# Performance work log

Hardware: AMD Instinct MI355X
Metric: run time of the kernel (lower is better)

## Reference

```python
import jax, jax.numpy as jnp
import numpy as np

B, S, D, H, F = 2, 2048, 1024, 16, 4096
DH = D // H  # per-head dim = 64
EPS = 1e-5


def _layer_norm(x, g, b):
    mu = jnp.mean(x, axis=-1, keepdims=True)
    var = jnp.mean((x - mu) ** 2, axis=-1, keepdims=True)
    return (x - mu) * jax.lax.rsqrt(var + EPS) * g + b


def _mha(q_in, kv_in, wq, bq, wk, bk, wv, bv, wo, bo, causal):
    b, s, d = q_in.shape
    q = (q_in @ wq + bq).reshape(b, s, H, DH).transpose(0, 2, 1, 3)
    k = (kv_in @ wk + bk).reshape(b, s, H, DH).transpose(0, 2, 1, 3)
    v = (kv_in @ wv + bv).reshape(b, s, H, DH).transpose(0, 2, 1, 3)
    scores = jnp.einsum('bhqd,bhkd->bhqk', q, k) / np.sqrt(DH).astype(np.float32)
    if causal:
        mask = jnp.tril(jnp.ones((s, s), dtype=bool))
        scores = jnp.where(mask, scores, -jnp.inf)
    attn = jax.nn.softmax(scores, axis=-1)
    out = jnp.einsum('bhqk,bhkd->bhqd', attn, v)
    out = out.transpose(0, 2, 1, 3).reshape(b, s, d)
    return out @ wo + bo


def setup_inputs() -> dict:
    key = jax.random.key(0)
    ks = iter(jax.random.split(key, 24))
    def w(shape, fan_in):
        return jax.random.normal(next(ks), shape, jnp.float32) / np.sqrt(fan_in).astype(np.float32)
    inp = {
        'encoder_output': jax.random.normal(next(ks), (B, S, D), jnp.float32),
        'decoder_input': jax.random.normal(next(ks), (B, S, D), jnp.float32),
    }
    for pre in ('sa', 'ca'):
        for nm in ('wq', 'wk', 'wv', 'wo'):
            inp[f'{pre}_{nm}'] = w((D, D), D)
            inp[f'{pre}_b{nm[-1]}'] = jnp.zeros((D,), jnp.float32)
        inp[f'{pre}_g'] = jnp.ones((D,), jnp.float32)
        inp[f'{pre}_bt'] = jnp.zeros((D,), jnp.float32)
    inp['f_w1'] = w((D, F), D); inp['f_b1'] = jnp.zeros((F,), jnp.float32)
    inp['f_w2'] = w((F, D), F); inp['f_b2'] = jnp.zeros((D,), jnp.float32)
    inp['f_g'] = jnp.ones((D,), jnp.float32); inp['f_bt'] = jnp.zeros((D,), jnp.float32)
    return inp


def reference(encoder_output, decoder_input,
              sa_wq, sa_bq, sa_wk, sa_bk, sa_wv, sa_bv, sa_wo, sa_bo, sa_g, sa_bt,
              ca_wq, ca_bq, ca_wk, ca_bk, ca_wv, ca_bv, ca_wo, ca_bo, ca_g, ca_bt,
              f_w1, f_b1, f_w2, f_b2, f_g, f_bt):
    # masked self-attention + residual + LN
    x = _mha(decoder_input, decoder_input, sa_wq, sa_bq, sa_wk, sa_bk, sa_wv, sa_bv, sa_wo, sa_bo, True)
    x = _layer_norm(x + decoder_input, sa_g, sa_bt)
    # encoder-decoder attention + residual + LN
    y = _mha(x, encoder_output, ca_wq, ca_bq, ca_wk, ca_bk, ca_wv, ca_bv, ca_wo, ca_bo, False)
    y = _layer_norm(y + x, ca_g, ca_bt)
    # FFN + residual + LN
    h = jax.nn.relu(y @ f_w1 + f_b1) @ f_w2 + f_b2
    return _layer_norm(h + y, f_g, f_bt)
```

## Files before the change

kernel.cpp:

```cpp
#include <hip/hip_runtime.h>
#include <hip/hip_bf16.h>


typedef __attribute__((ext_vector_type(8))) short bf16x8;
typedef __attribute__((ext_vector_type(4))) float f32x4;

#define LOG2E 1.44269504088896340736f

constexpr int Bb = 2, Ss = 2048, Dd = 1024, Hh = 16, DHd = 64, Ff = 4096;
constexpr int Mrows = Bb * Ss;
constexpr int BHS = Bb * Hh * Ss;

static __device__ __forceinline__ ushort f2b(float f) {
    union { float f; unsigned u; } x{f};
    unsigned r = x.u + 0x7fffu + ((x.u >> 16) & 1u);
    return (ushort)(r >> 16);
}

static __device__ __forceinline__ unsigned pk2(float a, float b) {
    __hip_bfloat162 h = __float22bfloat162_rn(make_float2(a, b));
    unsigned u;
    __builtin_memcpy(&u, &h, 4);
    return u;
}

static __device__ __forceinline__ unsigned pk2t(float a, float b) {
    union { float f; unsigned u; } ua{a}, ub{b};
    return __builtin_amdgcn_perm(ub.u, ua.u, 0x07060302);
}

static __device__ __forceinline__ void gl2lds16(const void* g, void* l) {
    __builtin_amdgcn_global_load_lds(
        (const __attribute__((address_space(1))) void*)g,
        (__attribute__((address_space(3))) void*)l, 16, 0, 0);
}

__global__ __launch_bounds__(256) void cvt_kernel(const float* __restrict__ in,
                                                  ushort* __restrict__ out) {
    int i = (blockIdx.x * 256 + threadIdx.x) * 4;
    float4 v = *(const float4*)(in + i);
    ushort4 u;
    u.x = f2b(v.x); u.y = f2b(v.y); u.z = f2b(v.z); u.w = f2b(v.w);
    *(ushort4*)(out + i) = u;
}

__global__ __launch_bounds__(256) void wtrans_kernel(const float* __restrict__ w,
                                                     ushort* __restrict__ wT,
                                                     int K, int N) {
    __shared__ float t[32][33];
    int tx = threadIdx.x & 31, ty = threadIdx.x >> 5;
    int kb = blockIdx.y * 32, nb = blockIdx.x * 32;
#pragma unroll
    for (int i = 0; i < 4; i++)
        t[ty + i * 8][tx] = w[(size_t)(kb + ty + i * 8) * N + nb + tx];
    __syncthreads();
#pragma unroll
    for (int i = 0; i < 4; i++)
        wT[(size_t)(nb + ty + i * 8) * K + kb + tx] = f2b(t[tx][ty + i * 8]);
}

__global__ __launch_bounds__(256) void pack_bias(const float* __restrict__ a,
                                                 const float* __restrict__ b,
                                                 const float* __restrict__ c,
                                                 float* __restrict__ out) {
    int i = blockIdx.x * 256 + threadIdx.x;
    const float* src = a; int j = i;
    if (i >= 2048)      { src = c; j = i - 2048; }
    else if (i >= 1024) { src = b; j = i - 1024; }
    out[i] = src[j];
}

__global__ __launch_bounds__(256) void gemm_kernel(const ushort* __restrict__ A,
                                                   const ushort* __restrict__ BT,
                                                   const float* __restrict__ bias,
                                                   void* __restrict__ out,
                                                   int M, int N, int K, int klen,
                                                   int mode, int relu, float qsc,
                                                   int vwhich) {
    __shared__ __align__(16) ushort As[128 * 64];
    __shared__ __align__(16) ushort Bs[128 * 64];
    const int tid = threadIdx.x;
    const int lane = tid & 63, wave = tid >> 6;
    const int lr = lane & 15, quad = lane >> 4;
    const int wm = wave & 1, wn = wave >> 1;
    const int m0 = blockIdx.y * 128, n0 = blockIdx.x * 128;
    const int kz = blockIdx.z;
    const int kstart = kz * klen;

    f32x4 acc[4][4];
#pragma unroll
    for (int i = 0; i < 4; i++)
#pragma unroll
        for (int j = 0; j < 4; j++) acc[i][j] = (f32x4){0.f, 0.f, 0.f, 0.f};

    const int srow = tid >> 3;
    const int gchunk = ((tid & 7) ^ (srow & 7)) * 8;
    const ushort* aBase = A + (size_t)(m0 + srow) * K + gchunk;
    const ushort* bBase = BT + (size_t)(n0 + srow) * K + gchunk;
    const size_t rowStep = (size_t)32 * K;

    const int slotA = ((quad) ^ (lr & 7)) * 8;
    const int slotB = ((4 + quad) ^ (lr & 7)) * 8;

    for (int k0 = kstart; k0 < kstart + klen; k0 += 64) {
#pragma unroll
        for (int c = 0; c < 4; c++) {
            gl2lds16(aBase + c * rowStep + k0, &As[c * 2048 + tid * 8]);
            gl2lds16(bBase + c * rowStep + k0, &Bs[c * 2048 + tid * 8]);
        }
        __syncthreads();
#pragma unroll
        for (int kk = 0; kk < 2; kk++) {
            const int slot = kk ? slotB : slotA;
            bf16x8 af[4], bfr[4];
#pragma unroll
            for (int i = 0; i < 4; i++)
                af[i] = *(const bf16x8*)&As[(wm * 64 + i * 16 + lr) * 64 + slot];
#pragma unroll
            for (int j = 0; j < 4; j++)
                bfr[j] = *(const bf16x8*)&Bs[(wn * 64 + j * 16 + lr) * 64 + slot];
#pragma unroll
            for (int i = 0; i < 4; i++)
#pragma unroll
                for (int j = 0; j < 4; j++)
                    acc[i][j] = __builtin_amdgcn_mfma_f32_16x16x32_bf16(af[i], bfr[j], acc[i][j], 0, 0, 0);
        }
        __syncthreads();
    }

#pragma unroll
    for (int j = 0; j < 4; j++) {
        int col = n0 + wn * 64 + j * 16 + lr;
        float bv = (bias && kz == 0) ? bias[col] : 0.f;
#pragma unroll
        for (int i = 0; i < 4; i++) {
            int row0 = m0 + wm * 64 + i * 16 + quad * 4;
            float v[4];
#pragma unroll
            for (int r = 0; r < 4; r++) {
                v[r] = acc[i][j][r] + bv;
                if (relu) v[r] = fmaxf(v[r], 0.f);
            }
            if (mode == 0) {
                float* op = (float*)out + (size_t)kz * M * N;
#pragma unroll
                for (int r = 0; r < 4; r++)
                    op[(size_t)(row0 + r) * N + col] = v[r];
            } else if (mode == 1) {
#pragma unroll
                for (int r = 0; r < 4; r++)
                    ((ushort*)out)[(size_t)(row0 + r) * N + col] = f2b(v[r]);
            } else {
                int which = col >> 10, n1 = col & 1023;
                int h = n1 >> 6, dh = n1 & 63;
                int b = row0 >> 11, s0 = row0 & 2047;
                size_t wbase = (size_t)which * (Bb * Hh * Ss * DHd);
                if (which == vwhich) {
                    uint2 pk;
                    pk.x = pk2(v[0], v[1]); pk.y = pk2(v[2], v[3]);
                    *(uint2*)((ushort*)out + wbase +
                              ((size_t)(b * Hh + h) * DHd + dh) * Ss + s0) = pk;
                } else {
                    float sc = (which == 0) ? qsc : 1.f;
#pragma unroll
                    for (int r = 0; r < 4; r++)
                        ((ushort*)out)[wbase + (((size_t)(b * Hh + h) * Ss + s0 + r) * DHd) + dh] =
                            f2b(v[r] * sc);
                }
            }
        }
    }
}

__global__ __launch_bounds__(256, 5) void attn_kernel(const ushort* __restrict__ Q,
                                                      const ushort* __restrict__ Kg,
                                                      const ushort* __restrict__ VT,
                                                      float* __restrict__ Op0,
                                                      float* __restrict__ Op1,
                                                      float* __restrict__ Ml,
                                                      int causal) {
    __shared__ ushort Ks[64][72];
    __shared__ ushort Vs[64][72];
    __shared__ ushort Ps[4][16][72];
    const int tid = threadIdx.x;
    const int lane = tid & 63, w = tid >> 6;
    const int lr = lane & 15, quad = lane >> 4;
    const int p = blockIdx.z;
    const int qt = causal ? (gridDim.x - 1 - blockIdx.x) : blockIdx.x;
    const int bh = blockIdx.y;
    const size_t hb = (size_t)bh * Ss * DHd;
    const int qrow = qt * 64 + w * 16;
    const int qg = qrow + lr;

    bf16x8 qf0 = *(const bf16x8*)(Q + hb + (size_t)qg * DHd + quad * 8);
    bf16x8 qf1 = *(const bf16x8*)(Q + hb + (size_t)qg * DHd + 32 + quad * 8);

    f32x4 o[4];
#pragma unroll
    for (int d = 0; d < 4; d++) o[d] = (f32x4){0.f, 0.f, 0.f, 0.f};
    float l_i = 0.f;

    const int srow = tid >> 3, sseg = tid & 7;

    const int ktEnd = causal ? (qt + 1) : (Ss / 64);
    for (int kt = p; kt < ktEnd; kt += 2) {
        const int k0 = kt * 64;
#pragma unroll
        for (int io = 0; io < 2; io++) {
            *(bf16x8*)&Ks[srow + io * 32][sseg * 8] =
                *(const bf16x8*)(Kg + hb + (size_t)(k0 + srow + io * 32) * DHd + sseg * 8);
            *(bf16x8*)&Vs[srow + io * 32][sseg * 8] =
                *(const bf16x8*)(VT + hb + (size_t)(srow + io * 32) * Ss + k0 + sseg * 8);
        }
        __syncthreads();

        f32x4 st[4];
#pragma unroll
        for (int k16 = 0; k16 < 4; k16++) {
            bf16x8 a0 = *(const bf16x8*)&Ks[k16 * 16 + lr][quad * 8];
            bf16x8 a1 = *(const bf16x8*)&Ks[k16 * 16 + lr][32 + quad * 8];
            f32x4 z = (f32x4){0.f, 0.f, 0.f, 0.f};
            z = __builtin_amdgcn_mfma_f32_16x16x32_bf16(a0, qf0, z, 0, 0, 0);
            st[k16] = __builtin_amdgcn_mfma_f32_16x16x32_bf16(a1, qf1, z, 0, 0, 0);
        }
        if (causal && kt == qt) {
#pragma unroll
            for (int k16 = 0; k16 < 4; k16++)
#pragma unroll
                for (int r = 0; r < 4; r++) {
                    int key = k0 + k16 * 16 + quad * 4 + r;
                    if (key > qg) st[k16][r] = -1e30f;
                }
        }
        float pv[4][4], psum = 0.f;
#pragma unroll
        for (int k16 = 0; k16 < 4; k16++)
#pragma unroll
            for (int r = 0; r < 4; r++) {
                pv[k16][r] = __builtin_amdgcn_exp2f(fminf(st[k16][r], 88.f));
                psum += pv[k16][r];
            }
        psum += __shfl_xor(psum, 16);
        psum += __shfl_xor(psum, 32);
        l_i += psum;
#pragma unroll
        for (int k16 = 0; k16 < 4; k16++) {
            uint2 pk;
            pk.x = pk2t(pv[k16][0], pv[k16][1]);
            pk.y = pk2t(pv[k16][2], pv[k16][3]);
            *(uint2*)&Ps[w][lr][k16 * 16 + quad * 4] = pk;
        }
#pragma unroll
        for (int kh = 0; kh < 2; kh++) {
            bf16x8 pb = *(const bf16x8*)&Ps[w][lr][kh * 32 + quad * 8];
#pragma unroll
            for (int dt = 0; dt < 4; dt++) {
                bf16x8 av = *(const bf16x8*)&Vs[dt * 16 + lr][kh * 32 + quad * 8];
                o[dt] = __builtin_amdgcn_mfma_f32_16x16x32_bf16(av, pb, o[dt], 0, 0, 0);
            }
        }
        __syncthreads();
    }

    float* Op = p ? Op1 : Op0;
    if (quad == 0)
        Ml[(size_t)p * BHS + (size_t)bh * Ss + qg] = l_i;
    size_t ob = ((size_t)bh * Ss + qg) * 64;
#pragma unroll
    for (int dt = 0; dt < 4; dt++)
        *(f32x4*)(Op + ob + dt * 16 + quad * 4) = o[dt];
}

__global__ __launch_bounds__(256) void attn_combine(const float* __restrict__ Op0,
                                                    const float* __restrict__ Op1,
                                                    const float* __restrict__ Ml,
                                                    ushort* __restrict__ O) {
    int g = blockIdx.x * 256 + threadIdx.x;
    int q = g >> 4, seg = g & 15;
    float inv = 1.f / (Ml[q] + Ml[BHS + q]);
    f32x4 x = *(const f32x4*)(Op0 + (size_t)q * 64 + seg * 4);
    f32x4 y = *(const f32x4*)(Op1 + (size_t)q * 64 + seg * 4);
    int bh = q >> 11, sq = q & 2047, bb = bh >> 4, h = bh & 15;
    uint2 u;
    u.x = pk2((x[0] + y[0]) * inv, (x[1] + y[1]) * inv);
    u.y = pk2((x[2] + y[2]) * inv, (x[3] + y[3]) * inv);
    *(uint2*)(O + ((size_t)(bb * Ss + sq)) * Dd + h * 64 + seg * 4) = u;
}

__global__ __launch_bounds__(256) void ln_kernel(const float* __restrict__ a0,
                                                 const float* __restrict__ a1,
                                                 const float* __restrict__ a2,
                                                 const float* __restrict__ a3,
                                                 const float* __restrict__ resid,
                                                 const float* __restrict__ g,
                                                 const float* __restrict__ bt,
                                                 float* __restrict__ out32,
                                                 ushort* __restrict__ outb) {
    const int row = blockIdx.x, tid = threadIdx.x;
    const size_t base = (size_t)row * Dd + tid * 4;
    float4 av = *(const float4*)(a0 + base);
    if (a1) { float4 t = *(const float4*)(a1 + base); av.x += t.x; av.y += t.y; av.z += t.z; av.w += t.w; }
    if (a2) { float4 t = *(const float4*)(a2 + base); av.x += t.x; av.y += t.y; av.z += t.z; av.w += t.w; }
    if (a3) { float4 t = *(const float4*)(a3 + base); av.x += t.x; av.y += t.y; av.z += t.z; av.w += t.w; }
    float4 rv = *(const float4*)(resid + base);
    float x0 = av.x + rv.x, x1 = av.y + rv.y, x2 = av.z + rv.z, x3 = av.w + rv.w;
    float s = x0 + x1 + x2 + x3;
    float q = x0 * x0 + x1 * x1 + x2 * x2 + x3 * x3;
#pragma unroll
    for (int off = 1; off <= 32; off <<= 1) {
        s += __shfl_xor(s, off);
        q += __shfl_xor(q, off);
    }
    __shared__ float red[8];
    int wave = tid >> 6, lane = tid & 63;
    if (lane == 0) { red[wave] = s; red[4 + wave] = q; }
    __syncthreads();
    s = red[0] + red[1] + red[2] + red[3];
    q = red[4] + red[5] + red[6] + red[7];
    float mu = s * (1.f / Dd);
    float var = q * (1.f / Dd) - mu * mu;
    float rs = rsqrtf(var + 1e-5f);
    int col = tid * 4;
    float4 gv = *(const float4*)(g + col);
    float4 bv = *(const float4*)(bt + col);
    float y0 = (x0 - mu) * rs * gv.x + bv.x;
    float y1 = (x1 - mu) * rs * gv.y + bv.y;
    float y2 = (x2 - mu) * rs * gv.z + bv.z;
    float y3 = (x3 - mu) * rs * gv.w + bv.w;
    if (out32) *(float4*)(out32 + base) = make_float4(y0, y1, y2, y3);
    if (outb) {
        ushort4 u; u.x = f2b(y0); u.y = f2b(y1); u.z = f2b(y2); u.w = f2b(y3);
        *(ushort4*)(outb + base) = u;
    }
}

constexpr size_t OFF_XB     = 0;
constexpr size_t OFF_ENCB   = OFF_XB     + 8388608;
constexpr size_t OFF_QKVWT  = OFF_ENCB   + 8388608;
constexpr size_t OFF_CAWQT  = OFF_QKVWT  + 6291456;
constexpr size_t OFF_CAKVT  = OFF_CAWQT  + 2097152;
constexpr size_t OFF_SAWOT  = OFF_CAKVT  + 4194304;
constexpr size_t OFF_CAWOT  = OFF_SAWOT  + 2097152;
constexpr size_t OFF_FW1T   = OFF_CAWOT  + 2097152;
constexpr size_t OFF_FW2T   = OFF_FW1T   + 8388608;
constexpr size_t OFF_SABQKV = OFF_FW2T   + 8388608;
constexpr size_t OFF_CABKV  = OFF_SABQKV + 12288;
constexpr size_t OFF_QB     = OFF_CABKV  + 8192;
constexpr size_t OFF_KB     = OFF_QB     + 8388608;
constexpr size_t OFF_VB     = OFF_KB     + 8388608;
constexpr size_t OFF_ATTNO  = OFF_VB     + 8388608;
constexpr size_t OFF_F1     = OFF_ATTNO  + 8388608;
constexpr size_t OFF_F2     = OFF_F1     + 16777216;
constexpr size_t OFF_X1B    = OFF_F2     + 16777216;
constexpr size_t OFF_F3     = OFF_X1B    + 8388608;
constexpr size_t OFF_YB     = OFF_F3     + 16777216;
constexpr size_t OFF_H1B    = OFF_YB     + 8388608;

extern "C" void kernel_launch(void* const* d_in, const int* in_sizes, int n_in,
                              void* d_out, int out_size, void* d_ws, size_t ws_size,
                              hipStream_t stream) {
    const float* enc   = (const float*)d_in[0];
    const float* dec   = (const float*)d_in[1];
    const float* sa_wq = (const float*)d_in[2];
    const float* sa_bq = (const float*)d_in[3];
    const float* sa_wk = (const float*)d_in[4];
    const float* sa_bk = (const float*)d_in[5];
    const float* sa_wv = (const float*)d_in[6];
    const float* sa_bv = (const float*)d_in[7];
    const float* sa_wo = (const float*)d_in[8];
    const float* sa_bo = (const float*)d_in[9];
    const float* sa_g  = (const float*)d_in[10];
    const float* sa_bt = (const float*)d_in[11];
    const float* ca_wq = (const float*)d_in[12];
    const float* ca_bq = (const float*)d_in[13];
    const float* ca_wk = (const float*)d_in[14];
    const float* ca_bk = (const float*)d_in[15];
    const float* ca_wv = (const float*)d_in[16];
    const float* ca_bv = (const float*)d_in[17];
    const float* ca_wo = (const float*)d_in[18];
    const float* ca_bo = (const float*)d_in[19];
    const float* ca_g  = (const float*)d_in[20];
    const float* ca_bt = (const float*)d_in[21];
    const float* f_w1  = (const float*)d_in[22];
    const float* f_b1  = (const float*)d_in[23];
    const float* f_w2  = (const float*)d_in[24];
    const float* f_b2  = (const float*)d_in[25];
    const float* f_g   = (const float*)d_in[26];
    const float* f_bt  = (const float*)d_in[27];

    char* ws = (char*)d_ws;
    ushort* xb     = (ushort*)(ws + OFF_XB);
    ushort* encb   = (ushort*)(ws + OFF_ENCB);
    ushort* qkvwT  = (ushort*)(ws + OFF_QKVWT);
    ushort* cawqT  = (ushort*)(ws + OFF_CAWQT);
    ushort* cakvT  = (ushort*)(ws + OFF_CAKVT);
    ushort* sawoT  = (ushort*)(ws + OFF_SAWOT);
    ushort* cawoT  = (ushort*)(ws + OFF_CAWOT);
    ushort* fw1T   = (ushort*)(ws + OFF_FW1T);
    ushort* fw2T   = (ushort*)(ws + OFF_FW2T);
    float*  sabqkv = (float*)(ws + OFF_SABQKV);
    float*  cabkv  = (float*)(ws + OFF_CABKV);
    ushort* qb     = (ushort*)(ws + OFF_QB);
    ushort* kb     = (ushort*)(ws + OFF_KB);
    ushort* vbt    = (ushort*)(ws + OFF_VB);
    ushort* attno  = (ushort*)(ws + OFF_ATTNO);
    float*  f1     = (float*)(ws + OFF_F1);
    float*  f2     = (float*)(ws + OFF_F2);
    ushort* x1b    = (ushort*)(ws + OFF_X1B);
    float*  x1f    = (float*)(ws + OFF_F3);
    ushort* yb     = (ushort*)(ws + OFF_YB);
    ushort* h1b    = (ushort*)(ws + OFF_H1B);
    float*  yfp    = (float*)(ws + OFF_QB);
    float*  ml     = (float*)(ws + OFF_H1B);

    const float QSC = 0.125f * LOG2E;
    const size_t MN = (size_t)Mrows * Dd;

    cvt_kernel<<<4096, 256, 0, stream>>>(dec, xb);
    cvt_kernel<<<4096, 256, 0, stream>>>(enc, encb);
    dim3 tgDD(32, 32);
    wtrans_kernel<<<tgDD, 256, 0, stream>>>(sa_wq, qkvwT,                 Dd, Dd);
    wtrans_kernel<<<tgDD, 256, 0, stream>>>(sa_wk, qkvwT + 1024 * 1024,   Dd, Dd);
    wtrans_kernel<<<tgDD, 256, 0, stream>>>(sa_wv, qkvwT + 2 * 1024 * 1024, Dd, Dd);
    wtrans_kernel<<<tgDD, 256, 0, stream>>>(sa_wo, sawoT,                 Dd, Dd);
    wtrans_kernel<<<tgDD, 256, 0, stream>>>(ca_wq, cawqT,                 Dd, Dd);
    wtrans_kernel<<<tgDD, 256, 0, stream>>>(ca_wk, cakvT,                 Dd, Dd);
    wtrans_kernel<<<tgDD, 256, 0, stream>>>(ca_wv, cakvT + 1024 * 1024,   Dd, Dd);
    wtrans_kernel<<<tgDD, 256, 0, stream>>>(ca_wo, cawoT,                 Dd, Dd);
    wtrans_kernel<<<dim3(128, 32), 256, 0, stream>>>(f_w1, fw1T, Dd, Ff);
    wtrans_kernel<<<dim3(32, 128), 256, 0, stream>>>(f_w2, fw2T, Ff, Dd);
    pack_bias<<<12, 256, 0, stream>>>(sa_bq, sa_bk, sa_bv, sabqkv);
    pack_bias<<<8, 256, 0, stream>>>(ca_bk, ca_bv, nullptr, cabkv);

    gemm_kernel<<<dim3(24, 32, 1), 256, 0, stream>>>(xb, qkvwT, sabqkv, qb,
                                                     Mrows, 3072, Dd, Dd, 2, 0, QSC, 2);
    attn_kernel<<<dim3(32, 32, 2), 256, 0, stream>>>(qb, kb, vbt, f1, x1f, ml, 1);
    attn_combine<<<4096, 256, 0, stream>>>(f1, x1f, ml, attno);
    gemm_kernel<<<dim3(8, 32, 2), 256, 0, stream>>>(attno, sawoT, sa_bo, f1,
                                                    Mrows, Dd, Dd, 512, 0, 0, 1.f, -1);
    ln_kernel<<<4096, 256, 0, stream>>>(f1, f2, nullptr, nullptr, dec,
                                        sa_g, sa_bt, x1f, x1b);

    gemm_kernel<<<dim3(8, 32, 1), 256, 0, stream>>>(x1b, cawqT, ca_bq, qb,
                                                    Mrows, Dd, Dd, Dd, 2, 0, QSC, -1);
    gemm_kernel<<<dim3(16, 32, 1), 256, 0, stream>>>(encb, cakvT, cabkv, kb,
                                                     Mrows, 2048, Dd, Dd, 2, 0, 1.f, 1);
    attn_kernel<<<dim3(32, 32, 2), 256, 0, stream>>>(qb, kb, vbt, f1, f2, ml, 0);
    attn_combine<<<4096, 256, 0, stream>>>(f1, f2, ml, attno);
    gemm_kernel<<<dim3(8, 32, 2), 256, 0, stream>>>(attno, cawoT, ca_bo, f1,
                                                    Mrows, Dd, Dd, 512, 0, 0, 1.f, -1);
    ln_kernel<<<4096, 256, 0, stream>>>(f1, f2, nullptr, nullptr, x1f,
                                        ca_g, ca_bt, yfp, yb);

    gemm_kernel<<<dim3(32, 32, 1), 256, 0, stream>>>(yb, fw1T, f_b1, h1b,
                                                     Mrows, Ff, Dd, Dd, 1, 1, 1.f, -1);
    gemm_kernel<<<dim3(8, 32, 4), 256, 0, stream>>>(h1b, fw2T, f_b2, f1,
                                                    Mrows, Dd, Ff, 1024, 0, 0, 1.f, -1);
    ln_kernel<<<4096, 256, 0, stream>>>(f1, f1 + MN, f1 + 2 * MN, f1 + 3 * MN, yfp,
                                        f_g, f_bt, (float*)d_out, nullptr);
}
```

Baseline: 619.3 us.

## Rewrite attention with 256-row query tiles and 32x32x16 MFMA, register-resident P

The attention kernel now handles 256 query rows per block, 64 per wave, instead of 64. It uses 32x32x16 bf16 MFMAs and keeps the probability tile in registers via v_permlane32_swap instead of staging it through LDS. K/V tiles are loaded with direct global-to-LDS copies into an XOR-swizzled layout, and causal split blocks are paired in reverse order to balance work. The goal is more K/V reuse per LDS load and fewer LDS round trips, at the cost of more registers, lower occupancy (launch bound 2) and a 4x smaller grid.

```diff
diff --git a/kernel.cpp b/kernel.cpp
--- a/kernel.cpp
+++ b/kernel.cpp
@@ -4,6 +4,7 @@
 
 typedef __attribute__((ext_vector_type(8))) short bf16x8;
 typedef __attribute__((ext_vector_type(4))) float f32x4;
+typedef __attribute__((ext_vector_type(16))) float f32x16;
 
 #define LOG2E 1.44269504088896340736f
 
@@ -172,103 +173,142 @@
     }
 }
 
-__global__ __launch_bounds__(256, 5) void attn_kernel(const ushort* __restrict__ Q,
+__global__ __launch_bounds__(256, 2) void attn_kernel(const ushort* __restrict__ Q,
                                                       const ushort* __restrict__ Kg,
                                                       const ushort* __restrict__ VT,
                                                       float* __restrict__ Op0,
                                                       float* __restrict__ Op1,
                                                       float* __restrict__ Ml,
                                                       int causal) {
-    __shared__ ushort Ks[64][72];
-    __shared__ ushort Vs[64][72];
-    __shared__ ushort Ps[4][16][72];
+    __shared__ __align__(16) ushort Ks[64 * 64];
+    __shared__ __align__(16) ushort Vs[64 * 64];
     const int tid = threadIdx.x;
     const int lane = tid & 63, w = tid >> 6;
-    const int lr = lane & 15, quad = lane >> 4;
+    const int lr31 = lane & 31, hi = lane >> 5, l7 = lane & 7;
+    const int hi4 = hi * 4;
     const int p = blockIdx.z;
-    const int qt = causal ? (gridDim.x - 1 - blockIdx.x) : blockIdx.x;
+    const int qt = causal ? (p ? blockIdx.x : (gridDim.x - 1 - blockIdx.x))
+                          : blockIdx.x;
     const int bh = blockIdx.y;
     const size_t hb = (size_t)bh * Ss * DHd;
-    const int qrow = qt * 64 + w * 16;
-    const int qg = qrow + lr;
-
-    bf16x8 qf0 = *(const bf16x8*)(Q + hb + (size_t)qg * DHd + quad * 8);
-    bf16x8 qf1 = *(const bf16x8*)(Q + hb + (size_t)qg * DHd + 32 + quad * 8);
-
-    f32x4 o[4];
-#pragma unroll
-    for (int d = 0; d < 4; d++) o[d] = (f32x4){0.f, 0.f, 0.f, 0.f};
-    float l_i = 0.f;
-
-    const int srow = tid >> 3, sseg = tid & 7;
-
-    const int ktEnd = causal ? (qt + 1) : (Ss / 64);
+    const int qbase = qt * 256 + w * 64;
+
+    bf16x8 qf[2][4];
+#pragma unroll
+    for (int qg = 0; qg < 2; qg++)
+#pragma unroll
+        for (int ks = 0; ks < 4; ks++)
+            qf[qg][ks] = *(const bf16x8*)(Q + hb +
+                (size_t)(qbase + qg * 32 + lr31) * DHd + ks * 16 + hi * 8);
+
+    f32x16 o[2][2];
+#pragma unroll
+    for (int i = 0; i < 2; i++)
+#pragma unroll
+        for (int j = 0; j < 2; j++)
+#pragma unroll
+            for (int r = 0; r < 16; r++) o[i][j][r] = 0.f;
+    float l0 = 0.f, l1 = 0.f;
+
+    const int srow8 = tid >> 3, sslot = tid & 7;
+    const int sswz = (sslot ^ (srow8 & 7)) * 8;
+    const ushort* kSrc = Kg + hb + (size_t)srow8 * DHd + sswz;
+    const ushort* vSrc = VT + hb + (size_t)srow8 * Ss + sswz;
+
+    int so[4];
+#pragma unroll
+    for (int ks = 0; ks < 4; ks++) so[ks] = ((ks * 2 + hi) ^ l7) * 8;
+
+    const int ktEnd = causal ? (qt + 1) * 4 : (Ss / 64);
     for (int kt = p; kt < ktEnd; kt += 2) {
         const int k0 = kt * 64;
 #pragma unroll
-        for (int io = 0; io < 2; io++) {
-            *(bf16x8*)&Ks[srow + io * 32][sseg * 8] =
-                *(const bf16x8*)(Kg + hb + (size_t)(k0 + srow + io * 32) * DHd + sseg * 8);
-            *(bf16x8*)&Vs[srow + io * 32][sseg * 8] =
-                *(const bf16x8*)(VT + hb + (size_t)(srow + io * 32) * Ss + k0 + sseg * 8);
+        for (int c = 0; c < 2; c++) {
+            gl2lds16(kSrc + (size_t)(k0 + c * 32) * DHd, &Ks[c * 2048 + tid * 8]);
+            gl2lds16(vSrc + (size_t)(c * 32) * Ss + k0, &Vs[c * 2048 + tid * 8]);
         }
         __syncthreads();
-
-        f32x4 st[4];
-#pragma unroll
-        for (int k16 = 0; k16 < 4; k16++) {
-            bf16x8 a0 = *(const bf16x8*)&Ks[k16 * 16 + lr][quad * 8];
-            bf16x8 a1 = *(const bf16x8*)&Ks[k16 * 16 + lr][32 + quad * 8];
-            f32x4 z = (f32x4){0.f, 0.f, 0.f, 0.f};
-            z = __builtin_amdgcn_mfma_f32_16x16x32_bf16(a0, qf0, z, 0, 0, 0);
-            st[k16] = __builtin_amdgcn_mfma_f32_16x16x32_bf16(a1, qf1, z, 0, 0, 0);
-        }
-        if (causal && kt == qt) {
-#pragma unroll
-            for (int k16 = 0; k16 < 4; k16++)
-#pragma unroll
-                for (int r = 0; r < 4; r++) {
-                    int key = k0 + k16 * 16 + quad * 4 + r;
-                    if (key > qg) st[k16][r] = -1e30f;
+        if (!causal || k0 <= qbase + 63) {
+            bf16x8 pb[2][4];
+            float ps0 = 0.f, ps1 = 0.f;
+            const int maskT = causal && (k0 == qbase);
+#pragma unroll
+            for (int kg = 0; kg < 2; kg++) {
+                bf16x8 kf[4];
+#pragma unroll
+                for (int ks = 0; ks < 4; ks++)
+                    kf[ks] = *(const bf16x8*)&Ks[(kg * 32 + lr31) * 64 + so[ks]];
+                f32x16 st[2];
+#pragma unroll
+                for (int qg = 0; qg < 2; qg++) {
+#pragma unroll
+                    for (int r = 0; r < 16; r++) st[qg][r] = 0.f;
+#pragma unroll
+                    for (int ks = 0; ks < 4; ks++)
+                        st[qg] = __builtin_amdgcn_mfma_f32_32x32x16_bf16(
+                            kf[ks], qf[qg][ks], st[qg], 0, 0, 0);
                 }
-        }
-        float pv[4][4], psum = 0.f;
-#pragma unroll
-        for (int k16 = 0; k16 < 4; k16++)
-#pragma unroll
-            for (int r = 0; r < 4; r++) {
-                pv[k16][r] = __builtin_amdgcn_exp2f(fminf(st[k16][r], 88.f));
-                psum += pv[k16][r];
+                if (maskT) {
+#pragma unroll
+                    for (int r = 0; r < 16; r++) {
+                        int klr = kg * 32 + (r & 3) + 8 * (r >> 2) + hi4;
+                        st[0][r] = (klr > lr31) ? -1e30f : st[0][r];
+                        st[1][r] = (klr > lr31 + 32) ? -1e30f : st[1][r];
+                    }
+                }
+#pragma unroll
+                for (int qg = 0; qg < 2; qg++) {
+                    float pv[16];
+#pragma unroll
+                    for (int r = 0; r < 16; r++) {
+                        pv[r] = __builtin_amdgcn_exp2f(fminf(st[qg][r], 88.f));
+                        if (qg == 0) ps0 += pv[r]; else ps1 += pv[r];
+                    }
+#pragma unroll
+                    for (int t = 0; t < 2; t++) {
+                        const int rb = t * 8;
+                        unsigned X0 = pk2t(pv[rb + 0], pv[rb + 1]);
+                        unsigned X1 = pk2t(pv[rb + 2], pv[rb + 3]);
+                        unsigned Y0 = pk2t(pv[rb + 4], pv[rb + 5]);
+                        unsigned Y1 = pk2t(pv[rb + 6], pv[rb + 7]);
+                        asm("v_permlane32_swap_b32 %0, %1" : "+v"(X0), "+v"(Y0));
+                        asm("v_permlane32_swap_b32 %0, %1" : "+v"(X1), "+v"(Y1));
+                        union { unsigned u[4]; bf16x8 v; } pw;
+                        pw.u[0] = X0; pw.u[1] = X1; pw.u[2] = Y0; pw.u[3] = Y1;
+                        pb[qg][kg * 2 + t] = pw.v;
+                    }
+                }
             }
-        psum += __shfl_xor(psum, 16);
-        psum += __shfl_xor(psum, 32);
-        l_i += psum;
-#pragma unroll
-        for (int k16 = 0; k16 < 4; k16++) {
-            uint2 pk;
-            pk.x = pk2t(pv[k16][0], pv[k16][1]);
-            pk.y = pk2t(pv[k16][2], pv[k16][3]);
-            *(uint2*)&Ps[w][lr][k16 * 16 + quad * 4] = pk;
-        }
-#pragma unroll
-        for (int kh = 0; kh < 2; kh++) {
-            bf16x8 pb = *(const bf16x8*)&Ps[w][lr][kh * 32 + quad * 8];
-#pragma unroll
-            for (int dt = 0; dt < 4; dt++) {
-                bf16x8 av = *(const bf16x8*)&Vs[dt * 16 + lr][kh * 32 + quad * 8];
-                o[dt] = __builtin_amdgcn_mfma_f32_16x16x32_bf16(av, pb, o[dt], 0, 0, 0);
+            l0 += ps0 + __shfl_xor(ps0, 32);
+            l1 += ps1 + __shfl_xor(ps1, 32);
+#pragma unroll
+            for (int ks = 0; ks < 4; ks++) {
+                bf16x8 av0 = *(const bf16x8*)&Vs[lr31 * 64 + so[ks]];
+                bf16x8 av1 = *(const bf16x8*)&Vs[(32 + lr31) * 64 + so[ks]];
+                o[0][0] = __builtin_amdgcn_mfma_f32_32x32x16_bf16(av0, pb[0][ks], o[0][0], 0, 0, 0);
+                o[0][1] = __builtin_amdgcn_mfma_f32_32x32x16_bf16(av1, pb[0][ks], o[0][1], 0, 0, 0);
+                o[1][0] = __builtin_amdgcn_mfma_f32_32x32x16_bf16(av0, pb[1][ks], o[1][0], 0, 0, 0);
+                o[1][1] = __builtin_amdgcn_mfma_f32_32x32x16_bf16(av1, pb[1][ks], o[1][1], 0, 0, 0);
             }
         }
         __syncthreads();
     }
 
+    Ml[(size_t)p * BHS + (size_t)bh * Ss + qbase + lane] = (lane & 32) ? l1 : l0;
     float* Op = p ? Op1 : Op0;
-    if (quad == 0)
-        Ml[(size_t)p * BHS + (size_t)bh * Ss + qg] = l_i;
-    size_t ob = ((size_t)bh * Ss + qg) * 64;
-#pragma unroll
-    for (int dt = 0; dt < 4; dt++)
-        *(f32x4*)(Op + ob + dt * 16 + quad * 4) = o[dt];
+#pragma unroll
+    for (int qg = 0; qg < 2; qg++) {
+        size_t ob = ((size_t)bh * Ss + qbase + qg * 32 + lr31) * 64;
+#pragma unroll
+        for (int dhg = 0; dhg < 2; dhg++)
+#pragma unroll
+            for (int rq = 0; rq < 4; rq++) {
+                f32x4 t;
+#pragma unroll
+                for (int c = 0; c < 4; c++) t[c] = o[qg][dhg][rq * 4 + c];
+                *(f32x4*)(Op + ob + dhg * 32 + rq * 8 + hi4) = t;
+            }
+    }
 }
 
 __global__ __launch_bounds__(256) void attn_combine(const float* __restrict__ Op0,
@@ -434,7 +474,7 @@
 
     gemm_kernel<<<dim3(24, 32, 1), 256, 0, stream>>>(xb, qkvwT, sabqkv, qb,
                                                      Mrows, 3072, Dd, Dd, 2, 0, QSC, 2);
-    attn_kernel<<<dim3(32, 32, 2), 256, 0, stream>>>(qb, kb, vbt, f1, x1f, ml, 1);
+    attn_kernel<<<dim3(8, 32, 2), 256, 0, stream>>>(qb, kb, vbt, f1, x1f, ml, 1);
     attn_combine<<<4096, 256, 0, stream>>>(f1, x1f, ml, attno);
     gemm_kernel<<<dim3(8, 32, 2), 256, 0, stream>>>(attno, sawoT, sa_bo, f1,
                                                     Mrows, Dd, Dd, 512, 0, 0, 1.f, -1);
@@ -445,7 +485,7 @@
                                                     Mrows, Dd, Dd, Dd, 2, 0, QSC, -1);
     gemm_kernel<<<dim3(16, 32, 1), 256, 0, stream>>>(encb, cakvT, cabkv, kb,
                                                      Mrows, 2048, Dd, Dd, 2, 0, 1.f, 1);
-    attn_kernel<<<dim3(32, 32, 2), 256, 0, stream>>>(qb, kb, vbt, f1, f2, ml, 0);
+    attn_kernel<<<dim3(8, 32, 2), 256, 0, stream>>>(qb, kb, vbt, f1, f2, ml, 0);
     attn_combine<<<4096, 256, 0, stream>>>(f1, f2, ml, attno);
     gemm_kernel<<<dim3(8, 32, 2), 256, 0, stream>>>(attno, cawoT, ca_bo, f1,
                                                     Mrows, Dd, Dd, 512, 0, 0, 1.f, -1);
```

Measured after the change: 576.4 us. 6.9% less time.
